# Kernel tuning notes

Measured on AMD Instinct MI355X. Metric: run time of the kernel, lower is better.

Reference implementation:

```python
import jax, jax.numpy as jnp
import numpy as np
from jax.scipy.special import logsumexp
from functools import partial

B, A, DIN, H, OUT, L = 256, 64, 512, 1024, 256, 3
HH = H // 2
SINKHORN_ITERS = 50
IDP = 0.1          # identity_preserve
SIG_BOUND = 1.0    # signal_bound
TEMP = 1.0
EPS = 1e-5


def setup_inputs() -> dict:
    key = jax.random.key(0)
    ks = iter(jax.random.split(key, 32))
    n = lambda shape, s=0.02: jax.random.normal(next(ks), shape, jnp.float32) * s
    return {
        'agent_states': jax.random.normal(next(ks), (B, A, DIN), jnp.float32),
        'Win': n((DIN, H), 0.03), 'bin_': jnp.zeros((H,), jnp.float32),
        # per-MHC-layer params, stacked over L
        'ln_g': jnp.ones((L, H), jnp.float32), 'ln_b': jnp.zeros((L, H), jnp.float32),
        'Wq': n((L, H, H)), 'bq': jnp.zeros((L, H), jnp.float32),
        'Wk': n((L, H, H)), 'bk': jnp.zeros((L, H), jnp.float32),
        'Wv': n((L, H, H)), 'bv': jnp.zeros((L, H), jnp.float32),
        'agent_biases': n((L, A, H)),
        'scale_factors': jnp.ones((L, A), jnp.float32),
        # inter-layer LayerNorms (L-1 of them)
        'iln_g': jnp.ones((L - 1, H), jnp.float32), 'iln_b': jnp.zeros((L - 1, H), jnp.float32),
        # per-agent output heads
        'W1': n((A, H, HH), 0.03), 'b1': jnp.zeros((A, HH), jnp.float32),
        'W2': n((A, HH, OUT), 0.03), 'b2': jnp.zeros((A, OUT), jnp.float32),
    }


def layer_norm(x, g, b):
    mu = jnp.mean(x, axis=-1, keepdims=True)
    var = jnp.mean(jnp.square(x - mu), axis=-1, keepdims=True)
    return (x - mu) * jax.lax.rsqrt(var + EPS) * g + b


def sinkhorn(log_alpha):
    # 50 alternating row/col log-space normalizations -> doubly stochastic
    def body(_, la):
        la = la - logsumexp(la, axis=2, keepdims=True)
        la = la - logsumexp(la, axis=1, keepdims=True)
        return la
    return jnp.exp(jax.lax.fori_loop(0, SINKHORN_ITERS, body, log_alpha))


def mhc_layer(h, ln_g, ln_b, Wq, bq, Wk, bk, Wv, bv, ab, sf):
    ns = layer_norm(h, ln_g, ln_b)                      # [B,A,H]
    q = ns @ Wq + bq
    k = ns @ Wk + bk
    v = ns @ Wv + bv
    scores = jnp.einsum('bad,bcd->bac', q, k) / (jnp.sqrt(jnp.float32(H)) * TEMP)
    attn = sinkhorn(scores)                              # [B,A,A]
    attended = jnp.einsum('bac,bcd->bad', attn, v)
    mixed = IDP * ns + (1.0 - IDP) * attended
    scaled = (mixed + ab) * sf[:, None]                  # bias + per-agent scale
    norms = jnp.linalg.norm(scaled, axis=2, keepdims=True)
    bounded = scaled / jnp.maximum(1.0, norms / SIG_BOUND)
    return h + bounded


def reference(agent_states, Win, bin_, ln_g, ln_b, Wq, bq, Wk, bk, Wv, bv,
              agent_biases, scale_factors, iln_g, iln_b, W1, b1, W2, b2):
    h = agent_states @ Win + bin_                        # input_proj (dropout=eval no-op)
    for i in range(L):
        h = mhc_layer(h, ln_g[i], ln_b[i], Wq[i], bq[i], Wk[i], bk[i],
                      Wv[i], bv[i], agent_biases[i], scale_factors[i])
        if i < L - 1:
            h = layer_norm(h, iln_g[i], iln_b[i])
    # per-agent MLP heads, vectorized over agents
    y = jnp.einsum('bah,aho->bao', h, W1) + b1
    y = jax.nn.gelu(y, approximate=False)
    out = jnp.einsum('bah,aho->bao', y, W2) + b2         # [B,A,OUT]
    return out
```

## Files before the change

kernel.cpp:

```cpp
#include <hip/hip_runtime.h>
#include <hip/hip_bf16.h>
#include <math.h>

#define BB 256
#define AA 64
#define DIN 512
#define HH_ 1024
#define HHALF 512
#define OUTD 256
#define LL 3
#define ROWS (BB * AA)
#define HN ((long)ROWS * HH_)

typedef float f32x4 __attribute__((ext_vector_type(4)));
typedef __bf16 bf16x8 __attribute__((ext_vector_type(8)));
typedef __bf16 bf16x4 __attribute__((ext_vector_type(4)));

__device__ __forceinline__ void gld_lds16(const void* g, void* l) {
    __builtin_amdgcn_global_load_lds(
        (const __attribute__((address_space(1))) unsigned int*)g,
        (__attribute__((address_space(3))) unsigned int*)l, 16, 0, 0);
}

#define TK 32
template <int ACT, int OUT_BF16, int SWZ>
__global__ __launch_bounds__(256) void mfma_gemm(
    const __bf16* __restrict__ Abase, const __bf16* __restrict__ Btbase,
    const float* __restrict__ biasBase, float* __restrict__ Cf,
    __bf16* __restrict__ Cb,
    int M, int N, int K, int lda, int ldb, int ldc,
    long sA, long sB, long sBias, long sC)
{
    const int z = blockIdx.z;
    const __bf16* A  = Abase  + (long)z * sA;
    const __bf16* Bt = Btbase + (long)z * sB;
    const float* bias = biasBase + (long)z * sBias;

    int bx = blockIdx.x, by = blockIdx.y;
    if (SWZ) {
        int lid = by * 24 + bx;
        int xcd = lid & 7, s = lid >> 3;
        by = (xcd >> 1) * 32 + s / 12;
        bx = (xcd & 1) * 12 + s % 12;
    }
    const int m0 = by * 128;
    const int n0 = bx * 128;

    __shared__ __bf16 sAt[128 * TK];
    __shared__ __bf16 sBt[128 * TK];

    const int t    = threadIdx.x;
    const int wv   = t >> 6;
    const int lane = t & 63;
    const int quad = lane >> 4;
    const int lrow = lane & 15;
    const int wm = (wv >> 1) * 64;
    const int wn = (wv & 1) * 64;

    f32x4 acc[4][4] = {};

    const int sr = t >> 2;
    const int sk = (t & 3) * 8;
    __bf16* la0 = sAt + wv * 512;
    __bf16* la1 = sAt + 64 * TK + wv * 512;
    __bf16* lb0 = sBt + wv * 512;
    __bf16* lb1 = sBt + 64 * TK + wv * 512;

    for (int k0 = 0; k0 < K; k0 += TK) {
        gld_lds16(A  + (long)(m0 + sr)      * lda + k0 + sk, la0);
        gld_lds16(A  + (long)(m0 + 64 + sr) * lda + k0 + sk, la1);
        gld_lds16(Bt + (long)(n0 + sr)      * ldb + k0 + sk, lb0);
        gld_lds16(Bt + (long)(n0 + 64 + sr) * ldb + k0 + sk, lb1);
        __syncthreads();

        bf16x8 af[4], bfr[4];
#pragma unroll
        for (int i = 0; i < 4; ++i)
            af[i] = *(const bf16x8*)(sAt + (wm + i * 16 + lrow) * TK + quad * 8);
#pragma unroll
        for (int j = 0; j < 4; ++j)
            bfr[j] = *(const bf16x8*)(sBt + (wn + j * 16 + lrow) * TK + quad * 8);
#pragma unroll
        for (int i = 0; i < 4; ++i)
#pragma unroll
            for (int j = 0; j < 4; ++j)
                acc[i][j] = __builtin_amdgcn_mfma_f32_16x16x32_bf16(
                    af[i], bfr[j], acc[i][j], 0, 0, 0);
        __syncthreads();
    }

#pragma unroll
    for (int i = 0; i < 4; ++i) {
#pragma unroll
        for (int p = 0; p < 4; ++p) {
            const int m = m0 + wm + i * 16 + quad * 4 + p;
#pragma unroll
            for (int j = 0; j < 4; ++j) {
                const int n = n0 + wn + j * 16 + lrow;
                float val = acc[i][j][p] + bias[n];
                if (ACT == 1) val = 0.5f * val * (1.0f + erff(val * 0.70710678118654752f));
                if (OUT_BF16) Cb[(long)z * sC + (long)m * ldc + n] = (__bf16)val;
                else          Cf[(long)z * sC + (long)m * ldc + n] = val;
            }
        }
    }
}

__global__ __launch_bounds__(256) void cast_kernel(
    const float* __restrict__ in, __bf16* __restrict__ out)
{
    long i = ((long)blockIdx.x * 256 + threadIdx.x) * 4;
    float4 v = *(const float4*)(in + i);
    bf16x4 o = {(__bf16)v.x, (__bf16)v.y, (__bf16)v.z, (__bf16)v.w};
    *(bf16x4*)(out + i) = o;
}

__global__ __launch_bounds__(256) void transpose_cast_kernel(
    const float* __restrict__ in, __bf16* __restrict__ out,
    int R, int C, long sIn, long sOut)
{
    const float* src = in + (long)blockIdx.z * sIn;
    __bf16* dst = out + (long)blockIdx.z * sOut;
    __shared__ float tile[32][33];
    const int r0 = blockIdx.y * 32, c0 = blockIdx.x * 32;
    const int tx = threadIdx.x & 31, ty = threadIdx.x >> 5;
#pragma unroll
    for (int i = 0; i < 32; i += 8)
        tile[ty + i][tx] = src[(long)(r0 + ty + i) * C + c0 + tx];
    __syncthreads();
#pragma unroll
    for (int i = 0; i < 32; i += 8)
        dst[(long)(c0 + ty + i) * R + r0 + tx] = (__bf16)tile[tx][ty + i];
}

__global__ __launch_bounds__(256) void transpose_qkv_kernel(
    const float* __restrict__ Wq, const float* __restrict__ Wk,
    const float* __restrict__ Wv, __bf16* __restrict__ out)
{
    const int zz = blockIdx.z;
    const int layer = zz / 3, which = zz - layer * 3;
    const float* src = (which == 0 ? Wq : which == 1 ? Wk : Wv) + (long)layer * 1048576;
    __bf16* dst = out + (long)layer * 3145728 + (long)which * 1048576;
    __shared__ float tile[32][33];
    const int r0 = blockIdx.y * 32, c0 = blockIdx.x * 32;
    const int tx = threadIdx.x & 31, ty = threadIdx.x >> 5;
#pragma unroll
    for (int i = 0; i < 32; i += 8)
        tile[ty + i][tx] = src[(long)(r0 + ty + i) * 1024 + c0 + tx];
    __syncthreads();
#pragma unroll
    for (int i = 0; i < 32; i += 8)
        dst[(long)(c0 + ty + i) * 1024 + r0 + tx] = (__bf16)tile[tx][ty + i];
}

__global__ __launch_bounds__(256) void qkv_bias_kernel(
    const float* __restrict__ bq, const float* __restrict__ bk,
    const float* __restrict__ bv, float* __restrict__ ob)
{
    int i = blockIdx.x * 256 + threadIdx.x;
    if (i >= LL * 3072) return;
    int l = i / 3072, j = i - l * 3072;
    float v = (j < 1024) ? bq[l * 1024 + j]
            : (j < 2048) ? bk[l * 1024 + j - 1024]
                         : bv[l * 1024 + j - 2048];
    ob[i] = v;
}

__global__ __launch_bounds__(256) void ln_kernel(
    const __bf16* __restrict__ x, const float* __restrict__ g,
    const float* __restrict__ b, __bf16* __restrict__ outb)
{
    const int wv = threadIdx.x >> 6, lane = threadIdx.x & 63;
    const long row = blockIdx.x * 4 + wv;
    const __bf16* xr = x + row * HH_;
    float v[16];
    float s = 0.f, s2 = 0.f;
#pragma unroll
    for (int i = 0; i < 4; ++i) {
        bf16x4 vb = *(const bf16x4*)(xr + i * 256 + lane * 4);
#pragma unroll
        for (int j = 0; j < 4; ++j) {
            float f = (float)vb[j];
            v[i * 4 + j] = f; s += f; s2 += f * f;
        }
    }
#pragma unroll
    for (int m = 1; m < 64; m <<= 1) { s += __shfl_xor(s, m); s2 += __shfl_xor(s2, m); }
    float mu = s * (1.0f / 1024.0f);
    float var = s2 * (1.0f / 1024.0f) - mu * mu;
    float rstd = rsqrtf(var + 1e-5f);
    __bf16* orow = outb + row * HH_;
#pragma unroll
    for (int i = 0; i < 4; ++i) {
        float4 gv = *(const float4*)(g + i * 256 + lane * 4);
        float4 bv = *(const float4*)(b + i * 256 + lane * 4);
        bf16x4 ob = {(__bf16)((v[i*4+0] - mu) * rstd * gv.x + bv.x),
                     (__bf16)((v[i*4+1] - mu) * rstd * gv.y + bv.y),
                     (__bf16)((v[i*4+2] - mu) * rstd * gv.z + bv.z),
                     (__bf16)((v[i*4+3] - mu) * rstd * gv.w + bv.w)};
        *(bf16x4*)(orow + i * 256 + lane * 4) = ob;
    }
}

__global__ __launch_bounds__(256) void attn_kernel(
    const __bf16* __restrict__ qkv, __bf16* __restrict__ att)
{
    const int z = blockIdx.x;
    __shared__ __bf16 sQ[64 * 32];
    __shared__ __bf16 sK[64 * 32];
    __shared__ float la[64 * 65];
    __shared__ float ps[4][64];
    __shared__ __bf16 sP[64 * 68];
    __shared__ __bf16 sVT[64 * 68];

    const int t = threadIdx.x;
    const int wv = t >> 6, lane = t & 63;
    const int quad = lane >> 4, lrow = lane & 15;
    const int wm = (wv >> 1) * 32, wn = (wv & 1) * 32;

    {
        const int srow = t >> 2;
        const int skoff = (t & 3) * 8;
        __bf16* lq = sQ + wv * 512;
        __bf16* lk = sK + wv * 512;
        const __bf16* Q = qkv + (long)z * 64 * 3072;
        const __bf16* K = Q + 1024;

        f32x4 acc[2][2] = {};
        for (int k0 = 0; k0 < 1024; k0 += 32) {
            gld_lds16(Q + (long)srow * 3072 + k0 + skoff, lq);
            gld_lds16(K + (long)srow * 3072 + k0 + skoff, lk);
            __syncthreads();
            bf16x8 af[2], bfr[2];
#pragma unroll
            for (int i = 0; i < 2; ++i)
                af[i] = *(const bf16x8*)(sQ + (wm + i * 16 + lrow) * 32 + quad * 8);
#pragma unroll
            for (int j = 0; j < 2; ++j)
                bfr[j] = *(const bf16x8*)(sK + (wn + j * 16 + lrow) * 32 + quad * 8);
#pragma unroll
            for (int i = 0; i < 2; ++i)
#pragma unroll
                for (int j = 0; j < 2; ++j)
                    acc[i][j] = __builtin_amdgcn_mfma_f32_16x16x32_bf16(
                        af[i], bfr[j], acc[i][j], 0, 0, 0);
            __syncthreads();
        }
#pragma unroll
        for (int i = 0; i < 2; ++i)
#pragma unroll
            for (int p = 0; p < 4; ++p) {
                const int r = wm + i * 16 + quad * 4 + p;
#pragma unroll
                for (int j = 0; j < 2; ++j)
                    la[r * 65 + wn + j * 16 + lrow] = acc[i][j][p] * 0.03125f;
            }
        __syncthreads();
    }

    for (int it = 0; it < 50; ++it) {
        {
            float vr[16];
            float sum = 0.f;
#pragma unroll
            for (int i = 0; i < 16; ++i) vr[i] = la[lane * 65 + wv * 16 + i];
#pragma unroll
            for (int i = 0; i < 16; ++i) sum += __expf(vr[i]);
            ps[wv][lane] = sum;
            __syncthreads();
            float lse = __logf(ps[0][lane] + ps[1][lane] + ps[2][lane] + ps[3][lane]);
#pragma unroll
            for (int i = 0; i < 16; ++i) la[lane * 65 + wv * 16 + i] = vr[i] - lse;
            __syncthreads();
        }
        {
            float vr[16];
            float sum = 0.f;
#pragma unroll
            for (int i = 0; i < 16; ++i) vr[i] = la[(wv * 16 + i) * 65 + lane];
#pragma unroll
            for (int i = 0; i < 16; ++i) sum += __expf(vr[i]);
            ps[wv][lane] = sum;
            __syncthreads();
            float lse = __logf(ps[0][lane] + ps[1][lane] + ps[2][lane] + ps[3][lane]);
#pragma unroll
            for (int i = 0; i < 16; ++i) la[(wv * 16 + i) * 65 + lane] = vr[i] - lse;
            __syncthreads();
        }
    }

#pragma unroll
    for (int i = 0; i < 16; ++i) {
        int idx = t + i * 256;
        int r = idx >> 6, c = idx & 63;
        sP[r * 68 + c] = (__bf16)__expf(la[r * 65 + c]);
    }
    __syncthreads();

    const __bf16* V = qkv + (long)z * 64 * 3072 + 2048;
    const int vc = t >> 2;
    const int vn = (t & 3) * 16;
    for (int tile = 0; tile < 16; ++tile) {
        bf16x8 v0 = *(const bf16x8*)(V + (long)vc * 3072 + tile * 64 + vn);
        bf16x8 v1 = *(const bf16x8*)(V + (long)vc * 3072 + tile * 64 + vn + 8);
#pragma unroll
        for (int j = 0; j < 8; ++j) sVT[(vn + j) * 68 + vc] = v0[j];
#pragma unroll
        for (int j = 0; j < 8; ++j) sVT[(vn + 8 + j) * 68 + vc] = v1[j];
        __syncthreads();

        f32x4 pacc[2][2] = {};
#pragma unroll
        for (int kb = 0; kb < 2; ++kb) {
            bf16x8 af[2], bfr[2];
#pragma unroll
            for (int i = 0; i < 2; ++i) {
                const __bf16* p = sP + (wm + i * 16 + lrow) * 68 + kb * 32 + quad * 8;
                bf16x4 lo = *(const bf16x4*)p;
                bf16x4 hi = *(const bf16x4*)(p + 4);
                af[i] = bf16x8{lo[0], lo[1], lo[2], lo[3], hi[0], hi[1], hi[2], hi[3]};
            }
#pragma unroll
            for (int j = 0; j < 2; ++j) {
                const __bf16* p = sVT + (wn + j * 16 + lrow) * 68 + kb * 32 + quad * 8;
                bf16x4 lo = *(const bf16x4*)p;
                bf16x4 hi = *(const bf16x4*)(p + 4);
                bfr[j] = bf16x8{lo[0], lo[1], lo[2], lo[3], hi[0], hi[1], hi[2], hi[3]};
            }
#pragma unroll
            for (int i = 0; i < 2; ++i)
#pragma unroll
                for (int j = 0; j < 2; ++j)
                    pacc[i][j] = __builtin_amdgcn_mfma_f32_16x16x32_bf16(
                        af[i], bfr[j], pacc[i][j], 0, 0, 0);
        }
#pragma unroll
        for (int i = 0; i < 2; ++i)
#pragma unroll
            for (int p = 0; p < 4; ++p) {
                const int r = wm + i * 16 + quad * 4 + p;
#pragma unroll
                for (int j = 0; j < 2; ++j) {
                    const int n = tile * 64 + wn + j * 16 + lrow;
                    att[((long)z * 64 + r) * HH_ + n] = (__bf16)pacc[i][j][p];
                }
            }
        __syncthreads();
    }
}

__global__ __launch_bounds__(256) void mix_kernel(
    const __bf16* __restrict__ nsb_in, const __bf16* __restrict__ att,
    const float* __restrict__ ab, const float* __restrict__ sf,
    __bf16* __restrict__ h,
    const float* __restrict__ ig, const float* __restrict__ ib,
    const float* __restrict__ g2, const float* __restrict__ b2p, int doLN,
    __bf16* __restrict__ nsb_out)
{
    const int wv = threadIdx.x >> 6, lane = threadIdx.x & 63;
    const long row = blockIdx.x * 4 + wv;
    const int a = (int)(row & 63);
    const float sfa = sf[a];

    const __bf16* nr = nsb_in + row * HH_;
    const __bf16* ar = att + row * HH_;
    const float* abr = ab + (long)a * HH_;

    float sc[16];
    float nrm2 = 0.f;
#pragma unroll
    for (int i = 0; i < 4; ++i) {
        bf16x4 nv = *(const bf16x4*)(nr + i * 256 + lane * 4);
        bf16x4 av = *(const bf16x4*)(ar + i * 256 + lane * 4);
        float4 a4 = *(const float4*)(abr + i * 256 + lane * 4);
        float v0 = (0.1f * (float)nv[0] + 0.9f * (float)av[0] + a4.x) * sfa;
        float v1 = (0.1f * (float)nv[1] + 0.9f * (float)av[1] + a4.y) * sfa;
        float v2 = (0.1f * (float)nv[2] + 0.9f * (float)av[2] + a4.z) * sfa;
        float v3 = (0.1f * (float)nv[3] + 0.9f * (float)av[3] + a4.w) * sfa;
        sc[i*4+0] = v0; sc[i*4+1] = v1; sc[i*4+2] = v2; sc[i*4+3] = v3;
        nrm2 += v0 * v0 + v1 * v1 + v2 * v2 + v3 * v3;
    }
#pragma unroll
    for (int m = 1; m < 64; m <<= 1) nrm2 += __shfl_xor(nrm2, m);
    float norm = sqrtf(nrm2);
    float inv = norm > 1.0f ? 1.0f / norm : 1.0f;

    __bf16* hr = h + row * HH_;
    float hn[16];
    float s = 0.f, s2 = 0.f;
#pragma unroll
    for (int i = 0; i < 4; ++i) {
        bf16x4 hv = *(const bf16x4*)(hr + i * 256 + lane * 4);
#pragma unroll
        for (int j = 0; j < 4; ++j) {
            float f = (float)hv[j] + sc[i * 4 + j] * inv;
            hn[i * 4 + j] = f; s += f; s2 += f * f;
        }
    }
    if (!doLN) {
#pragma unroll
        for (int i = 0; i < 4; ++i) {
            bf16x4 ob = {(__bf16)hn[i*4+0], (__bf16)hn[i*4+1],
                         (__bf16)hn[i*4+2], (__bf16)hn[i*4+3]};
            *(bf16x4*)(hr + i * 256 + lane * 4) = ob;
        }
        return;
    }
#pragma unroll
    for (int m = 1; m < 64; m <<= 1) { s += __shfl_xor(s, m); s2 += __shfl_xor(s2, m); }
    float mu = s * (1.0f / 1024.0f);
    float var = s2 * (1.0f / 1024.0f) - mu * mu;
    float rstd = rsqrtf(var + 1e-5f);
    float s_1 = 0.f, s2_1 = 0.f;
#pragma unroll
    for (int i = 0; i < 4; ++i) {
        float4 gv = *(const float4*)(ig + i * 256 + lane * 4);
        float4 bv = *(const float4*)(ib + i * 256 + lane * 4);
        float f0 = (hn[i*4+0] - mu) * rstd * gv.x + bv.x;
        float f1 = (hn[i*4+1] - mu) * rstd * gv.y + bv.y;
        float f2 = (hn[i*4+2] - mu) * rstd * gv.z + bv.z;
        float f3 = (hn[i*4+3] - mu) * rstd * gv.w + bv.w;
        hn[i*4+0] = f0; hn[i*4+1] = f1; hn[i*4+2] = f2; hn[i*4+3] = f3;
        s_1 += f0 + f1 + f2 + f3;
        s2_1 += f0 * f0 + f1 * f1 + f2 * f2 + f3 * f3;
        bf16x4 ob = {(__bf16)f0, (__bf16)f1, (__bf16)f2, (__bf16)f3};
        *(bf16x4*)(hr + i * 256 + lane * 4) = ob;
    }
#pragma unroll
    for (int m = 1; m < 64; m <<= 1) { s_1 += __shfl_xor(s_1, m); s2_1 += __shfl_xor(s2_1, m); }
    mu = s_1 * (1.0f / 1024.0f);
    var = s2_1 * (1.0f / 1024.0f) - mu * mu;
    rstd = rsqrtf(var + 1e-5f);
    __bf16* nor = nsb_out + row * HH_;
#pragma unroll
    for (int i = 0; i < 4; ++i) {
        float4 gv = *(const float4*)(g2 + i * 256 + lane * 4);
        float4 bv = *(const float4*)(b2p + i * 256 + lane * 4);
        bf16x4 ob = {(__bf16)((hn[i*4+0] - mu) * rstd * gv.x + bv.x),
                     (__bf16)((hn[i*4+1] - mu) * rstd * gv.y + bv.y),
                     (__bf16)((hn[i*4+2] - mu) * rstd * gv.z + bv.z),
                     (__bf16)((hn[i*4+3] - mu) * rstd * gv.w + bv.w)};
        *(bf16x4*)(nor + i * 256 + lane * 4) = ob;
    }
}

extern "C" void kernel_launch(void* const* d_in, const int* in_sizes, int n_in,
                              void* d_out, int out_size, void* d_ws, size_t ws_size,
                              hipStream_t stream)
{
    const float* agent_states = (const float*)d_in[0];
    const float* Win   = (const float*)d_in[1];
    const float* bin_  = (const float*)d_in[2];
    const float* ln_g  = (const float*)d_in[3];
    const float* ln_b  = (const float*)d_in[4];
    const float* Wq    = (const float*)d_in[5];
    const float* bq    = (const float*)d_in[6];
    const float* Wk    = (const float*)d_in[7];
    const float* bk    = (const float*)d_in[8];
    const float* Wv    = (const float*)d_in[9];
    const float* bv    = (const float*)d_in[10];
    const float* ab    = (const float*)d_in[11];
    const float* sf    = (const float*)d_in[12];
    const float* ilg   = (const float*)d_in[13];
    const float* ilb   = (const float*)d_in[14];
    const float* W1    = (const float*)d_in[15];
    const float* b1    = (const float*)d_in[16];
    const float* W2    = (const float*)d_in[17];
    const float* b2    = (const float*)d_in[18];
    float* out = (float*)d_out;

    float* qbias = (float*)d_ws;
    __bf16* base = (__bf16*)(qbias + 16384);
    __bf16* nsb   = base;
    __bf16* h     = nsb + HN;
    __bf16* att   = h + HN;
    __bf16* qkvb  = att + HN;
    __bf16* Wqkvt = qkvb + 3 * HN;
    __bf16* asb  = att;
    __bf16* Wint = att + 8388608;
    __bf16* W1t = qkvb;
    __bf16* W2t = qkvb + 33554432;
    __bf16* yb  = qkvb + 41943040;

    cast_kernel<<<8192, 256, 0, stream>>>(agent_states, asb);
    transpose_cast_kernel<<<dim3(32, 16, 1), 256, 0, stream>>>(Win, Wint, 512, 1024, 0, 0);
    transpose_qkv_kernel<<<dim3(32, 32, 9), 256, 0, stream>>>(Wq, Wk, Wv, Wqkvt);
    qkv_bias_kernel<<<36, 256, 0, stream>>>(bq, bk, bv, qbias);

    mfma_gemm<0, 1, 0><<<dim3(8, 128, 1), 256, 0, stream>>>(
        asb, Wint, bin_, nullptr, h, ROWS, HH_, DIN, DIN, DIN, HH_, 0, 0, 0, 0);
    ln_kernel<<<ROWS / 4, 256, 0, stream>>>(h, ln_g, ln_b, nsb);

    for (int i = 0; i < LL; ++i) {
        mfma_gemm<0, 1, 1><<<dim3(24, 128, 1), 256, 0, stream>>>(
            nsb, Wqkvt + (long)i * 3145728, qbias + i * 3072, nullptr, qkvb,
            ROWS, 3072, HH_, HH_, HH_, 3072, 0, 0, 0, 0);
        attn_kernel<<<BB, 256, 0, stream>>>(qkvb, att);
        const int last = (i == LL - 1);
        mix_kernel<<<ROWS / 4, 256, 0, stream>>>(
            nsb, att, ab + (long)i * AA * HH_, sf + i * AA, h,
            ilg + (last ? 0 : i) * HH_, ilb + (last ? 0 : i) * HH_,
            ln_g + (last ? 0 : (i + 1)) * HH_, ln_b + (last ? 0 : (i + 1)) * HH_,
            last ? 0 : 1, nsb);
    }

    transpose_cast_kernel<<<dim3(16, 32, 64), 256, 0, stream>>>(W1, W1t, 1024, 512,
                                                                524288, 524288);
    transpose_cast_kernel<<<dim3(8, 16, 64), 256, 0, stream>>>(W2, W2t, 512, 256,
                                                               131072, 131072);
    mfma_gemm<1, 1, 0><<<dim3(4, 2, 64), 256, 0, stream>>>(
        h, W1t, b1, nullptr, yb, BB, HHALF, HH_,
        AA * HH_, HH_, AA * HHALF, HH_, (long)HHALF * HH_, HHALF, HHALF);
    mfma_gemm<0, 0, 0><<<dim3(2, 2, 64), 256, 0, stream>>>(
        yb, W2t, b2, out, nullptr, BB, OUTD, HHALF,
        AA * HHALF, HHALF, AA * OUTD, HHALF, (long)OUTD * HHALF, OUTD, OUTD);
}
```

Baseline: 1.130 ms.

## Add 256x256-tile double-buffered MFMA GEMM for input and QKV projections

Adds a new 512-thread GEMM kernel with 256x256 output tiles and 64-wide K steps. It double-buffers LDS with direct global-to-LDS loads, uses an XOR swizzle against bank conflicts, applies grid swizzling and raises wave priority during MFMA bursts. The input projection and the per-layer fused QKV GEMMs are switched to it, aiming for more data reuse per tile and better overlap of loads with compute. The cost is 128KB of LDS per block, which limits occupancy to one block per CU, plus a fragile hand-written vmcnt and barrier schedule.

```diff
diff --git a/kernel.cpp b/kernel.cpp
--- a/kernel.cpp
+++ b/kernel.cpp
@@ -20,6 +20,126 @@
     __builtin_amdgcn_global_load_lds(
         (const __attribute__((address_space(1))) unsigned int*)g,
         (__attribute__((address_space(3))) unsigned int*)l, 16, 0, 0);
+}
+
+__global__ __launch_bounds__(512) void mfma_gemm256(
+    const __bf16* __restrict__ A, const __bf16* __restrict__ Bt,
+    const float* __restrict__ bias, __bf16* __restrict__ C,
+    int K, int ldc)
+{
+    __shared__ __bf16 sA[2][256 * 64];
+    __shared__ __bf16 sB[2][256 * 64];
+
+    const int NT = K >> 6;
+    const int t = threadIdx.x;
+    const int wv = t >> 6;
+    const int lane = t & 63;
+    const int quad = lane >> 4;
+    const int lrow = lane & 15;
+    const int wr = wv >> 2;
+    const int wc = wv & 3;
+    const int swz = (lane & 7) << 3;
+    const int cs0 = (quad * 8) ^ swz;
+    const int cs1 = (32 + quad * 8) ^ swz;
+
+    const int nbx = gridDim.x;
+    const int nwg = nbx * gridDim.y;
+    const int flat = blockIdx.y * nbx + blockIdx.x;
+    const int s_ = (flat & 7) * (nwg >> 3) + (flat >> 3);
+    const int bx = s_ % nbx, by = s_ / nbx;
+    const int m0 = by * 256, n0 = bx * 256;
+
+    f32x4 acc[8][4] = {};
+    bf16x8 af[4][2], bLo[2][2], bHi[2][2];
+
+    auto STAGE = [&](int tt, int isB, int half) {
+        __bf16* region = (isB ? sB[tt & 1] : sA[tt & 1]) + half * 8192;
+        const __bf16* g = isB ? Bt : A;
+        const long row0 = (long)(isB ? n0 : m0) + half * 128;
+        const int k0 = tt << 6;
+#pragma unroll
+        for (int it = 0; it < 2; ++it) {
+            const int r = it * 64 + (t >> 3);
+            const int kc = (((t & 7) ^ (r & 7)) << 3);
+            gld_lds16(g + (row0 + r) * (long)K + k0 + kc,
+                      region + it * 4096 + wv * 512);
+        }
+    };
+    auto READ_A = [&](const __bf16* buf, int rb) {
+#pragma unroll
+        for (int fr = 0; fr < 4; ++fr) {
+            const __bf16* p = buf + (rb + fr * 16 + lrow) * 64;
+            af[fr][0] = *(const bf16x8*)(p + cs0);
+            af[fr][1] = *(const bf16x8*)(p + cs1);
+        }
+    };
+    auto READ_B = [&](bf16x8 (&bf)[2][2], const __bf16* buf, int rb) {
+#pragma unroll
+        for (int nf = 0; nf < 2; ++nf) {
+            const __bf16* p = buf + (rb + nf * 16 + lrow) * 64;
+            bf[nf][0] = *(const bf16x8*)(p + cs0);
+            bf[nf][1] = *(const bf16x8*)(p + cs1);
+        }
+    };
+    auto MF = [&](bf16x8 (&bf)[2][2], int mh, int nh) {
+        __builtin_amdgcn_s_setprio(1);
+#pragma unroll
+        for (int fr = 0; fr < 4; ++fr)
+#pragma unroll
+            for (int nf = 0; nf < 2; ++nf)
+#pragma unroll
+                for (int s = 0; s < 2; ++s)
+                    acc[mh * 4 + fr][nh * 2 + nf] =
+                        __builtin_amdgcn_mfma_f32_16x16x32_bf16(
+                            af[fr][s], bf[nf][s], acc[mh * 4 + fr][nh * 2 + nf],
+                            0, 0, 0);
+        __builtin_amdgcn_s_setprio(0);
+    };
+
+    STAGE(0, 0, 0); STAGE(0, 1, 0); STAGE(0, 0, 1); STAGE(0, 1, 1);
+    STAGE(1, 1, 0); STAGE(1, 0, 0);
+    asm volatile("s_waitcnt vmcnt(4)" ::: "memory");
+    __builtin_amdgcn_s_barrier();
+
+    for (int j = 0; j < NT; ++j) {
+        const __bf16* cA = sA[j & 1];
+        const __bf16* cB = sB[j & 1];
+        READ_A(cA, wr * 128);
+        READ_B(bLo, cB, wc * 64);
+        if (j + 1 < NT) STAGE(j + 1, 1, 1);
+        __builtin_amdgcn_s_barrier();
+        MF(bLo, 0, 0);
+        __builtin_amdgcn_s_barrier();
+        READ_B(bHi, cB, wc * 64 + 32);
+        if (j + 1 < NT) STAGE(j + 1, 0, 1);
+        __builtin_amdgcn_s_barrier();
+        MF(bHi, 0, 1);
+        __builtin_amdgcn_s_barrier();
+        READ_A(cA, wr * 128 + 64);
+        if (j + 2 < NT) STAGE(j + 2, 1, 0);
+        __builtin_amdgcn_s_barrier();
+        MF(bLo, 1, 0);
+        __builtin_amdgcn_s_barrier();
+        if (j + 2 < NT) STAGE(j + 2, 0, 0);
+        __builtin_amdgcn_s_barrier();
+        MF(bHi, 1, 1);
+        if (j < NT - 2)       asm volatile("s_waitcnt vmcnt(4)" ::: "memory");
+        else if (j == NT - 2) asm volatile("s_waitcnt vmcnt(0)" ::: "memory");
+        __builtin_amdgcn_s_barrier();
+    }
+
+#pragma unroll
+    for (int mi = 0; mi < 8; ++mi) {
+#pragma unroll
+        for (int p = 0; p < 4; ++p) {
+            const int m = m0 + wr * 128 + mi * 16 + quad * 4 + p;
+#pragma unroll
+            for (int ni = 0; ni < 4; ++ni) {
+                const int n = n0 + wc * 64 + ni * 16 + lrow;
+                C[(long)m * ldc + n] = (__bf16)(acc[mi][ni][p] + bias[n]);
+            }
+        }
+    }
 }
 
 #define TK 32
@@ -487,14 +607,12 @@
     transpose_qkv_kernel<<<dim3(32, 32, 9), 256, 0, stream>>>(Wq, Wk, Wv, Wqkvt);
     qkv_bias_kernel<<<36, 256, 0, stream>>>(bq, bk, bv, qbias);
 
-    mfma_gemm<0, 1, 0><<<dim3(8, 128, 1), 256, 0, stream>>>(
-        asb, Wint, bin_, nullptr, h, ROWS, HH_, DIN, DIN, DIN, HH_, 0, 0, 0, 0);
+    mfma_gemm256<<<dim3(4, 64), 512, 0, stream>>>(asb, Wint, bin_, h, DIN, HH_);
     ln_kernel<<<ROWS / 4, 256, 0, stream>>>(h, ln_g, ln_b, nsb);
 
     for (int i = 0; i < LL; ++i) {
-        mfma_gemm<0, 1, 1><<<dim3(24, 128, 1), 256, 0, stream>>>(
-            nsb, Wqkvt + (long)i * 3145728, qbias + i * 3072, nullptr, qkvb,
-            ROWS, 3072, HH_, HH_, HH_, 3072, 0, 0, 0, 0);
+        mfma_gemm256<<<dim3(12, 64), 512, 0, stream>>>(
+            nsb, Wqkvt + (long)i * 3145728, qbias + i * 3072, qkvb, HH_, 3072);
         attn_kernel<<<BB, 256, 0, stream>>>(qkvb, att);
         const int last = (i == LL - 1);
         mix_kernel<<<ROWS / 4, 256, 0, stream>>>(
```

Result: faster. 1.019 ms (-9.8%).
